# Performance work log

Hardware: AMD Instinct MI355X
Metric: run time of the kernel (lower is better)

## Reference

```python
import jax, jax.numpy as jnp
import numpy as np

D_MODEL = 512; NHEAD = 8; D_FF = 2048
B = 8; C = 64; P = 128
HALF = D_MODEL // 2        # per-branch embed dim (256)
H_HALF = NHEAD // 2        # per-branch heads (4)
HD = HALF // H_HALF        # per-branch head dim (64)
ROPE_BASE = 10000.0
THETA_SCALE = 2.0 * np.pi
LN_EPS = 1e-5; RMS_EPS = 1e-8


def setup_inputs():
    ks = jax.random.split(jax.random.key(0), 16)
    w = lambda k, s: jax.random.normal(k, s, jnp.float32) * 0.02
    return {
        "src": jax.random.normal(ks[0], (B, C, P, D_MODEL), jnp.float32),
        "coords": jax.random.normal(ks[1], (C, 3), jnp.float32),
        "q_attn": w(ks[2], (D_MODEL,)), "rms_attn": jnp.ones((D_MODEL,), jnp.float32),
        "proj_attn_w": w(ks[3], (D_MODEL, D_MODEL)), "proj_attn_b": jnp.zeros((D_MODEL,), jnp.float32),
        "q_ffn": w(ks[4], (D_MODEL,)), "rms_ffn": jnp.ones((D_MODEL,), jnp.float32),
        "proj_ffn_w": w(ks[5], (D_MODEL, D_MODEL)), "proj_ffn_b": jnp.zeros((D_MODEL,), jnp.float32),
        "ln1_w": jnp.ones((D_MODEL,), jnp.float32), "ln1_b": jnp.zeros((D_MODEL,), jnp.float32),
        "ln2_w": jnp.ones((D_MODEL,), jnp.float32), "ln2_b": jnp.zeros((D_MODEL,), jnp.float32),
        "qkv_s_w": w(ks[6], (3 * HALF, HALF)), "qkv_s_b": jnp.zeros((3 * HALF,), jnp.float32),
        "out_s_w": w(ks[7], (HALF, HALF)), "out_s_b": jnp.zeros((HALF,), jnp.float32),
        "qkv_t_w": w(ks[8], (3 * HALF, HALF)), "qkv_t_b": jnp.zeros((3 * HALF,), jnp.float32),
        "out_t_w": w(ks[9], (HALF, HALF)), "out_t_b": jnp.zeros((HALF,), jnp.float32),
        "w1": w(ks[10], (D_FF, D_MODEL)), "b1": jnp.zeros((D_FF,), jnp.float32),
        "w2": w(ks[11], (D_MODEL, D_FF)), "b2": jnp.zeros((D_MODEL,), jnp.float32),
    }


def _rmsnorm(x, w):
    return x / jnp.sqrt(jnp.mean(x * x, axis=-1, keepdims=True) + RMS_EPS) * w


def _layernorm(x, w, b):
    m = jnp.mean(x, axis=-1, keepdims=True)
    v = jnp.mean((x - m) ** 2, axis=-1, keepdims=True)
    return (x - m) / jnp.sqrt(v + LN_EPS) * w + b


def _attn_residual(src, q, norm_w, proj_w, proj_b):
    # sources = [src] stacked on a leading n-axis (n=1) as in AttentionResidual
    V = src[None]                                  # (n, B, C, P, D)
    K = _rmsnorm(V, norm_w)
    logits = jnp.einsum('d,nbcpd->nbcp', q, K)
    wgt = jax.nn.softmax(logits, axis=0)
    out = jnp.einsum('nbcp,nbcpd->bcpd', wgt, V)
    return out @ proj_w.T + proj_b


def _build_freqs(half, dtype):
    idx = jnp.arange(half, dtype=dtype)
    return 1.0 / ROPE_BASE ** (idx / max(half, 1))


def _coord_rope(coords, half):
    # coords: (L, 3); returns cos, sin of shape (1, 1, L, half)
    axis_ids = jnp.arange(half) % 3
    c = coords - jnp.mean(coords, axis=0, keepdims=True)
    r = jnp.linalg.norm(c, axis=-1)
    c = c / jnp.maximum(jnp.max(r), 1e-6)
    freqs = _build_freqs(half, coords.dtype)
    theta = THETA_SCALE * (c[:, axis_ids] * freqs[None, :])   # (L, half)
    return jnp.cos(theta)[None, None], jnp.sin(theta)[None, None]


def _index_rope(L, half, dtype):
    freqs = _build_freqs(half, dtype)
    pos = jnp.arange(L, dtype=dtype)[:, None]
    theta = pos * freqs[None, :]                               # (L, half)
    return jnp.cos(theta)[None, None], jnp.sin(theta)[None, None]


def _apply_rope(q, k, cos, sin):
    half = q.shape[-1] // 2
    q1, q2 = q[..., :half], q[..., half:]
    k1, k2 = k[..., :half], k[..., half:]
    qr = jnp.concatenate([q1 * cos - q2 * sin, q1 * sin + q2 * cos], axis=-1)
    kr = jnp.concatenate([k1 * cos - k2 * sin, k1 * sin + k2 * cos], axis=-1)
    return qr, kr


def _mha(x, w_qkv, b_qkv, w_o, b_o, H, cos, sin):
    Bx, L, E = x.shape
    Hd = E // H
    qkv = x @ w_qkv.T + b_qkv
    q, k, v = jnp.split(qkv, 3, axis=-1)
    q = q.reshape(Bx, L, H, Hd).transpose(0, 2, 1, 3)   # (B, H, L, Hd)
    k = k.reshape(Bx, L, H, Hd).transpose(0, 2, 1, 3)
    v = v.reshape(Bx, L, H, Hd).transpose(0, 2, 1, 3)
    q, k = _apply_rope(q, k, cos, sin)
    scores = jnp.einsum('bhld,bhmd->bhlm', q, k) * (Hd ** -0.5)
    attn = jax.nn.softmax(scores, axis=-1)
    out = jnp.einsum('bhlm,bhmd->bhld', attn, v)
    out = out.transpose(0, 2, 1, 3).reshape(Bx, L, E)
    return out @ w_o.T + b_o


def reference(src, coords, q_attn, rms_attn, proj_attn_w, proj_attn_b,
              q_ffn, rms_ffn, proj_ffn_w, proj_ffn_b,
              ln1_w, ln1_b, ln2_w, ln2_b,
              qkv_s_w, qkv_s_b, out_s_w, out_s_b,
              qkv_t_w, qkv_t_b, out_t_w, out_t_b,
              w1, b1, w2, b2):
    Bx, Cx, Px, D = src.shape
    half = D // 2
    # --- attention block (pre-norm, attention-residual shortcut) ---
    res1 = _attn_residual(src, q_attn, rms_attn, proj_attn_w, proj_attn_b)
    x = _layernorm(src, ln1_w, ln1_b)
    # spatial branch: attention over channels with coordinate RoPE
    xs = x[..., :half].transpose(0, 2, 1, 3).reshape(Bx * Px, Cx, half)
    cos_s, sin_s = _coord_rope(coords, HD // 2)
    ys = _mha(xs, qkv_s_w, qkv_s_b, out_s_w, out_s_b, H_HALF, cos_s, sin_s)
    ys = ys.reshape(Bx, Px, Cx, half).transpose(0, 2, 1, 3)
    # temporal branch: attention over patches with index RoPE
    xt = x[..., half:].reshape(Bx * Cx, Px, half)
    cos_t, sin_t = _index_rope(Px, HD // 2, src.dtype)
    yt = _mha(xt, qkv_t_w, qkv_t_b, out_t_w, out_t_b, H_HALF, cos_t, sin_t)
    yt = yt.reshape(Bx, Cx, Px, half)
    x = res1 + jnp.concatenate([ys, yt], axis=-1)
    # --- FFN block ---
    res2 = _attn_residual(x, q_ffn, rms_ffn, proj_ffn_w, proj_ffn_b)
    y = _layernorm(x, ln2_w, ln2_b)
    ff = jax.nn.gelu(y @ w1.T + b1, approximate=False) @ w2.T + b2
    return res2 + ff
```

## Files before the change

kernel.cpp:

```cpp
#include <hip/hip_runtime.h>
#include <math.h>
#include <type_traits>

using u16 = unsigned short;
using u32 = unsigned int;

typedef __bf16 bf16x8 __attribute__((ext_vector_type(8)));
typedef float f32x4 __attribute__((ext_vector_type(4)));

__device__ __forceinline__ float lof(u32 u) { u32 x = u << 16; float f; __builtin_memcpy(&f, &x, 4); return f; }
__device__ __forceinline__ float hif(u32 u) { u32 x = u & 0xffff0000u; float f; __builtin_memcpy(&f, &x, 4); return f; }
__device__ __forceinline__ u16 f2bf(float f) {
  u32 u; __builtin_memcpy(&u, &f, 4);
  u32 r = u + 0x7fffu + ((u >> 16) & 1u);
  return (u16)(r >> 16);
}
__device__ __forceinline__ u32 pack2(float a, float b) { return (u32)f2bf(a) | ((u32)f2bf(b) << 16); }
__device__ __forceinline__ float bf2f(u16 s) { u32 x = ((u32)s) << 16; float f; __builtin_memcpy(&f, &x, 4); return f; }
__device__ __forceinline__ float elem(const u32* arr, int j) { u32 u = arr[j >> 1]; return (j & 1) ? hif(u) : lof(u); }

__device__ __forceinline__ void gload_lds16(const u16* g, u16* l) {
  __builtin_amdgcn_global_load_lds((const __attribute__((address_space(1))) void*)g,
                                   (__attribute__((address_space(3))) void*)l, 16, 0, 0);
}

#define NTOK 65536

#define WB_PA   0
#define WB_PF   262144
#define WB_QS   524288
#define WB_QT   720896
#define WB_OS   917504
#define WB_OT   983040
#define WB_W1   1048576
#define WB_W2F  2097152
#define WB_TOT  3407872

#define UC_US 0
#define UC_CS 768
#define UC_UT 1536
#define UC_CT 2304
#define UC_U1 3072
#define UC_C1 5120
#define UC_BC 7168

constexpr size_t O_WB  = 0;
constexpr size_t O_TAB = 6815744;
constexpr size_t O_ST1 = 6864896;
constexpr size_t O_ST2 = 7389184;
constexpr size_t O_UC  = 7913472;
constexpr size_t O_X   = 7944192;
constexpr size_t O_HB  = O_X + (size_t)NTOK * 512 * 2;

__global__ __launch_bounds__(256) void convert_weights_kernel(
    const float* __restrict__ pa, const float* __restrict__ pf,
    const float* __restrict__ qs, const float* __restrict__ qt,
    const float* __restrict__ os_, const float* __restrict__ ot,
    const float* __restrict__ w1, const float* __restrict__ w2,
    const float* __restrict__ ln1w, const float* __restrict__ ln2w,
    u16* __restrict__ dst)
{
  int i = blockIdx.x * 256 + threadIdx.x;
  if (i >= WB_TOT) return;
  float v;
  if (i < 262144)       { v = pa[i]; }
  else if (i < 524288)  { v = pf[i - 262144]; }
  else if (i < 720896)  { int l = i - 524288;  v = qs[l] * ln1w[l & 255]; }
  else if (i < 917504)  { int l = i - 720896;  v = qt[l] * ln1w[256 + (l & 255)]; }
  else if (i < 983040)  { v = os_[i - 917504]; }
  else if (i < 1048576) { v = ot[i - 983040]; }
  else if (i < 2097152) { int l = i - 1048576; v = w1[l] * ln2w[l & 511]; }
  else {
    int l = i - 2097152; int row = l / 2560, col = l - row * 2560;
    v = (col < 2048) ? w2[row * 2048 + col] : pf[row * 512 + (col - 2048)];
  }
  dst[i] = f2bf(v);
}

__global__ __launch_bounds__(256) void ucvec_kernel(
    const float* __restrict__ qs, const float* __restrict__ qt, const float* __restrict__ w1,
    const float* __restrict__ ln1w, const float* __restrict__ ln1b,
    const float* __restrict__ ln2w, const float* __restrict__ ln2b,
    const float* __restrict__ b2, const float* __restrict__ pfb,
    float* __restrict__ uc)
{
  int j = blockIdx.x * 256 + threadIdx.x;
  if (j < 768) {
    float u = 0.f, c = 0.f;
    for (int k = 0; k < 256; k++) { float w = qs[j * 256 + k]; u += ln1w[k] * w; c += ln1b[k] * w; }
    uc[UC_US + j] = u; uc[UC_CS + j] = c;
  } else if (j < 1536) {
    int jj = j - 768; float u = 0.f, c = 0.f;
    for (int k = 0; k < 256; k++) { float w = qt[jj * 256 + k]; u += ln1w[256 + k] * w; c += ln1b[256 + k] * w; }
    uc[UC_UT + jj] = u; uc[UC_CT + jj] = c;
  } else if (j < 3584) {
    int jj = j - 1536; float u = 0.f, c = 0.f;
    for (int k = 0; k < 512; k++) { float w = w1[jj * 512 + k]; u += ln2w[k] * w; c += ln2b[k] * w; }
    uc[UC_U1 + jj] = u; uc[UC_C1 + jj] = c;
  } else if (j < 4096) {
    int jj = j - 3584;
    uc[UC_BC + jj] = b2[jj] + pfb[jj];
  }
}

__global__ __launch_bounds__(256) void rope_tables_kernel(const float* __restrict__ coords, float* __restrict__ tab)
{
  __shared__ float cs[192];
  __shared__ float mean3[3];
  __shared__ float rmax;
  int t = threadIdx.x;
  if (t < 192) cs[t] = coords[t];
  __syncthreads();
  if (t < 3) { float s = 0.f; for (int i = 0; i < 64; i++) s += cs[i * 3 + t]; mean3[t] = s * (1.0f / 64.0f); }
  __syncthreads();
  if (t < 192) cs[t] -= mean3[t % 3];
  __syncthreads();
  if (t == 0) {
    float mx = 0.f;
    for (int i = 0; i < 64; i++) {
      float x = cs[i * 3], y = cs[i * 3 + 1], z = cs[i * 3 + 2];
      mx = fmaxf(mx, sqrtf(x * x + y * y + z * z));
    }
    rmax = fmaxf(mx, 1e-6f);
  }
  __syncthreads();
  float inv = 1.0f / rmax;
  for (int e = t; e < 2048; e += 256) {
    int c = e >> 5, j = e & 31;
    float freq = 1.0f / powf(10000.0f, (float)j * (1.0f / 32.0f));
    float th = 6.283185307179586f * (cs[c * 3 + (j % 3)] * inv) * freq;
    tab[e] = cosf(th); tab[2048 + e] = sinf(th);
  }
  for (int e = t; e < 4096; e += 256) {
    int p = e >> 5, j = e & 31;
    float freq = 1.0f / powf(10000.0f, (float)j * (1.0f / 32.0f));
    float th = (float)p * freq;
    tab[4096 + e] = cosf(th); tab[8192 + e] = sinf(th);
  }
}

__global__ __launch_bounds__(256) void ln_stats_f32_kernel(
    const float* __restrict__ xin, float2* __restrict__ st, u16* __restrict__ srcb)
{
  const int tok = blockIdx.x * 4 + (threadIdx.x >> 6);
  const int lane = threadIdx.x & 63;
  const float* row = xin + (size_t)tok * 512 + lane * 8;
  float4 v0 = ((const float4*)row)[0];
  float4 v1 = ((const float4*)row)[1];
  float v[8] = {v0.x, v0.y, v0.z, v0.w, v1.x, v1.y, v1.z, v1.w};
  float s = 0.f, ss = 0.f;
#pragma unroll
  for (int j = 0; j < 8; j++) { s += v[j]; ss += v[j] * v[j]; }
#pragma unroll
  for (int o = 32; o > 0; o >>= 1) { s += __shfl_xor(s, o); ss += __shfl_xor(ss, o); }
  if (lane == 0) {
    float mean = s * (1.0f / 512.0f);
    float rstd = rsqrtf(ss * (1.0f / 512.0f) - mean * mean + 1e-5f);
    st[tok] = make_float2(mean, rstd);
  }
  if (srcb) {
    uint4 o; u32* op = (u32*)&o;
#pragma unroll
    for (int d = 0; d < 4; d++) op[d] = pack2(v[2 * d], v[2 * d + 1]);
    *(uint4*)(srcb + (size_t)tok * 512 + lane * 8) = o;
  }
}

__global__ __launch_bounds__(256) void ln_stats_bf16_kernel(const u16* __restrict__ xin, float2* __restrict__ st)
{
  const int tok = blockIdx.x * 4 + (threadIdx.x >> 6);
  const int lane = threadIdx.x & 63;
  uint4 u = ((const uint4*)(xin + (size_t)tok * 512))[lane];
  u32 uu[4] = {u.x, u.y, u.z, u.w};
  float s = 0.f, ss = 0.f;
#pragma unroll
  for (int d = 0; d < 4; d++) {
    float a = lof(uu[d]), b = hif(uu[d]);
    s += a + b; ss += a * a + b * b;
  }
#pragma unroll
  for (int o = 32; o > 0; o >>= 1) { s += __shfl_xor(s, o); ss += __shfl_xor(ss, o); }
  if (lane == 0) {
    float mean = s * (1.0f / 512.0f);
    float rstd = rsqrtf(ss * (1.0f / 512.0f) - mean * mean + 1e-5f);
    st[tok] = make_float2(mean, rstd);
  }
}

#define BM 128
#define BN 128
#define BKT 32

template<int AMODE, int EMODE, typename OutT>
__global__ __launch_bounds__(256) void gemm_kernel(
    const void* __restrict__ Av, int lda,
    const u16* __restrict__ A2, int lda2,
    const u16* __restrict__ Wt, int ldw,
    OutT* __restrict__ C, int ldc,
    const float* __restrict__ bias,
    const float2* __restrict__ stats,
    const float* __restrict__ uvec, const float* __restrict__ cvec,
    int K)
{
  const int t = threadIdx.x;
  const int lane = t & 63, wid = t >> 6;
  const int wm = wid >> 1, wn = wid & 1;
  const int l15 = lane & 15, l4 = lane >> 4;
  const int r0 = t >> 2;

  const int ntn = gridDim.x;
  const int nwg = ntn * gridDim.y;
  int flat = blockIdx.y * ntn + blockIdx.x;
  int q = nwg >> 3, rmd = nwg & 7, xcd = flat & 7, idx = flat >> 3;
  int wg = (xcd < rmd ? xcd * (q + 1) : rmd * (q + 1) + (xcd - rmd) * q) + idx;
  const int m0 = (wg / ntn) * BM, n0 = (wg % ntn) * BN;

  f32x4 acc[4][4] = {};

  const size_t arow0 = (size_t)(m0 + r0);
  const u16* A16 = (const u16*)Av;
  const float* A32 = (const float*)Av;

  if constexpr (AMODE == 0 || AMODE == 4) {
    __shared__ u16 Asb[2][BM * 32];
    __shared__ u16 Bsb[2][BN * 32];
    const int chs = (t & 3) ^ ((t >> 3) & 3);
    const u16* Wp = Wt + (size_t)(n0 + r0) * ldw + chs * 8;
    const size_t wstep = (size_t)64 * ldw;
    const int nt = K / BKT;
    auto stage = [&](int ti, int buf) {
      const int kk = ti * BKT;
      const int cbk = kk + chs * 8;
      const u16* pa; size_t rstep;
      if constexpr (AMODE == 4) {
        if (kk < 2048) { pa = A16 + arow0 * lda + cbk;           rstep = (size_t)64 * lda; }
        else           { pa = A2 + arow0 * lda2 + (cbk - 2048);  rstep = (size_t)64 * lda2; }
      } else {
        pa = A16 + arow0 * lda + cbk; rstep = (size_t)64 * lda;
      }
      gload_lds16(pa, &Asb[buf][t * 8]);
      gload_lds16(pa + rstep, &Asb[buf][t * 8 + 2048]);
      gload_lds16(Wp + kk, &Bsb[buf][t * 8]);
      gload_lds16(Wp + wstep + kk, &Bsb[buf][t * 8 + 2048]);
    };
    stage(0, 0);
    int cur = 0;
    const int pco = (l4 ^ ((l15 >> 1) & 3)) * 8;
    for (int ti = 0; ti < nt; ti++) {
      if (ti + 1 < nt) {
        stage(ti + 1, cur ^ 1);
        __builtin_amdgcn_sched_barrier(0);
        asm volatile("s_waitcnt vmcnt(4)" ::: "memory");
      } else {
        __builtin_amdgcn_sched_barrier(0);
        asm volatile("s_waitcnt vmcnt(0)" ::: "memory");
      }
      __builtin_amdgcn_sched_barrier(0);
      __builtin_amdgcn_s_barrier();
      __builtin_amdgcn_sched_barrier(0);
      bf16x8 af[4], bfr[4];
#pragma unroll
      for (int i = 0; i < 4; i++)
        af[i] = *(const bf16x8*)(&Asb[cur][(wm * 64 + i * 16 + l15) * 32 + pco]);
#pragma unroll
      for (int j = 0; j < 4; j++)
        bfr[j] = *(const bf16x8*)(&Bsb[cur][(wn * 64 + j * 16 + l15) * 32 + pco]);
#pragma unroll
      for (int i = 0; i < 4; i++)
#pragma unroll
        for (int j = 0; j < 4; j++)
          acc[i][j] = __builtin_amdgcn_mfma_f32_16x16x32_bf16(af[i], bfr[j], acc[i][j], 0, 0, 0);
      __builtin_amdgcn_sched_barrier(0);
      __builtin_amdgcn_s_barrier();
      __builtin_amdgcn_sched_barrier(0);
      cur ^= 1;
    }
  } else {
    const int ch = t & 3;
    const u16* Wp = Wt + (size_t)(n0 + r0) * ldw + ch * 8;
    const size_t wstep = (size_t)64 * ldw;
    __shared__ u16 As[BM * 40];
    __shared__ u16 Bs[BN * 32];
    for (int k0 = 0; k0 < K; k0 += BKT) {
      const int cb = k0 + ch * 8;
      uint4 a0, a1;
      float f0[8], f1[8];
      float4 x0 = *(const float4*)(A32 + arow0 * lda + cb);
      float4 x1 = *(const float4*)(A32 + arow0 * lda + cb + 4);
      float4 y0 = *(const float4*)(A32 + (arow0 + 64) * lda + cb);
      float4 y1 = *(const float4*)(A32 + (arow0 + 64) * lda + cb + 4);
      f0[0]=x0.x; f0[1]=x0.y; f0[2]=x0.z; f0[3]=x0.w; f0[4]=x1.x; f0[5]=x1.y; f0[6]=x1.z; f0[7]=x1.w;
      f1[0]=y0.x; f1[1]=y0.y; f1[2]=y0.z; f1[3]=y0.w; f1[4]=y1.x; f1[5]=y1.y; f1[6]=y1.z; f1[7]=y1.w;
      u32* p0 = (u32*)&a0; u32* p1 = (u32*)&a1;
#pragma unroll
      for (int d = 0; d < 4; d++) { p0[d] = pack2(f0[2*d], f0[2*d+1]); p1[d] = pack2(f1[2*d], f1[2*d+1]); }
      __syncthreads();
      gload_lds16(Wp + k0, Bs + t * 8);
      gload_lds16(Wp + wstep + k0, Bs + t * 8 + 2048);
      *(uint4*)(As + r0 * 40 + ch * 8) = a0;
      *(uint4*)(As + (r0 + 64) * 40 + ch * 8) = a1;
      __syncthreads();
      bf16x8 af[4], bfr[4];
#pragma unroll
      for (int i = 0; i < 4; i++)
        af[i] = *(const bf16x8*)(As + (wm * 64 + i * 16 + l15) * 40 + l4 * 8);
#pragma unroll
      for (int j = 0; j < 4; j++)
        bfr[j] = *(const bf16x8*)(Bs + (wn * 64 + j * 16 + l15) * 32 + l4 * 8);
#pragma unroll
      for (int i = 0; i < 4; i++)
#pragma unroll
        for (int j = 0; j < 4; j++)
          acc[i][j] = __builtin_amdgcn_mfma_f32_16x16x32_bf16(af[i], bfr[j], acc[i][j], 0, 0, 0);
    }
  }

#pragma unroll
  for (int i = 0; i < 4; i++) {
    const int row = m0 + wm * 64 + i * 16 + l4 * 4;
#pragma unroll
    for (int j = 0; j < 4; j++) {
      const int col = n0 + wn * 64 + j * 16 + l15;
      const float bv = bias[col];
#pragma unroll
      for (int rr = 0; rr < 4; rr++) {
        float v = acc[i][j][rr];
        if constexpr (EMODE >= 3) {
          float2 s = stats[row + rr];
          v = s.y * v - s.x * s.y * uvec[col] + cvec[col] + bv;
          if constexpr (EMODE == 4) v = 0.5f * v * (1.0f + erff(v * 0.7071067811865475f));
        } else {
          v += bv;
        }
        const size_t idxc = (size_t)(row + rr) * ldc + col;
        if constexpr (std::is_same<OutT, u16>::value) {
          if constexpr (EMODE == 2) v += bf2f(C[idxc]);
          C[idxc] = f2bf(v);
        } else {
          if constexpr (EMODE == 2) v += C[idxc];
          C[idxc] = v;
        }
      }
    }
  }
}

template<int L>
__global__ __launch_bounds__(256) void attn_mfma_kernel(
    const u16* __restrict__ qkv,
    u16* __restrict__ aout,
    const float* __restrict__ tab)
{
  constexpr int KP = 72;
  constexpr int PP = L + 8;
  constexpr int VP = L + 8;
  constexpr int NI = L / 64;
  constexpr int NJ = L / 16;
  constexpr int NK = L / 32;
  __shared__ u16 Ks[L * KP];
  __shared__ u16 Vt[64 * VP];
  __shared__ u16 Ps[L * PP];

  const int t = threadIdx.x;
  const int lane = t & 63;
  const int w = t >> 6;
  const int l15 = lane & 15, l4 = lane >> 4;
  const int sq = blockIdx.x, h = blockIdx.y;

  long base; int tstride; const float *ct, *st;
  if constexpr (L == 64) { base = (long)(sq >> 7) * 8192 + (sq & 127); tstride = 128; ct = tab;        st = tab + 2048; }
  else                   { base = (long)sq * 128;                      tstride = 1;   ct = tab + 4096; st = tab + 8192; }

  {
    const int tok = t >> 1, hh = t & 1;
    if (tok < L) {
      const size_t rb = (size_t)(base + (long)tok * tstride) * 768 + h * 64;
      u32 ku[32];
#pragma unroll
      for (int i = 0; i < 8; i++) ((uint4*)ku)[i] = ((const uint4*)(qkv + rb + 256))[i];
      const float* cc = ct + tok * 32;
      const float* ss = st + tok * 32;
      u32* kd = (u32*)(Ks + tok * KP + hh * 32);
#pragma unroll
      for (int jj = 0; jj < 16; jj++) {
        float c0 = cc[2*jj], s0 = ss[2*jj], c1 = cc[2*jj+1], s1 = ss[2*jj+1];
        float a0 = elem(ku, 2*jj),     b0 = elem(ku, 2*jj+32);
        float a1 = elem(ku, 2*jj+1),   b1 = elem(ku, 2*jj+33);
        float r0v = hh ? (a0*s0 + b0*c0) : (a0*c0 - b0*s0);
        float r1v = hh ? (a1*s1 + b1*c1) : (a1*c1 - b1*s1);
        kd[jj] = pack2(r0v, r1v);
      }
      u32 vu[16];
#pragma unroll
      for (int i = 0; i < 4; i++) ((uint4*)vu)[i] = ((const uint4*)(qkv + rb + 512 + hh * 32))[i];
#pragma unroll
      for (int j = 0; j < 32; j++)
        Vt[(hh * 32 + j) * VP + tok] = (u16)(vu[j >> 1] >> ((j & 1) * 16));
    }
  }

  bf16x8 aq[NI][2];
#pragma unroll
  for (int i = 0; i < NI; i++) {
    const int row = w * (16 * NI) + i * 16 + l15;
    const u16* qr = qkv + (size_t)(base + (long)row * tstride) * 768 + h * 64;
    uint4 ua = *(const uint4*)(qr + l4 * 8);
    uint4 ub = *(const uint4*)(qr + 32 + l4 * 8);
    u32 au[4] = {ua.x, ua.y, ua.z, ua.w};
    u32 bu[4] = {ub.x, ub.y, ub.z, ub.w};
    const float* cc = ct + row * 32 + l4 * 8;
    const float* ss = st + row * 32 + l4 * 8;
    u32 q0[4], q1[4];
#pragma unroll
    for (int d = 0; d < 4; d++) {
      float a0 = lof(au[d]), a1 = hif(au[d]);
      float b0 = lof(bu[d]), b1 = hif(bu[d]);
      float c0 = cc[2*d], c1 = cc[2*d+1], s0 = ss[2*d], s1 = ss[2*d+1];
      q0[d] = pack2(a0*c0 - b0*s0, a1*c1 - b1*s1);
      q1[d] = pack2(a0*s0 + b0*c0, a1*s1 + b1*c1);
    }
    __builtin_memcpy(&aq[i][0], q0, 16);
    __builtin_memcpy(&aq[i][1], q1, 16);
  }
  __syncthreads();

  f32x4 acc[NI][NJ] = {};
#pragma unroll
  for (int j = 0; j < NJ; j++) {
#pragma unroll
    for (int kk = 0; kk < 2; kk++) {
      bf16x8 bk = *(const bf16x8*)(Ks + (j * 16 + l15) * KP + kk * 32 + l4 * 8);
#pragma unroll
      for (int i = 0; i < NI; i++)
        acc[i][j] = __builtin_amdgcn_mfma_f32_16x16x32_bf16(aq[i][kk], bk, acc[i][j], 0, 0, 0);
    }
  }

  float inv_[NI][4];
#pragma unroll
  for (int i = 0; i < NI; i++) {
#pragma unroll
    for (int rr = 0; rr < 4; rr++) {
      float m = acc[i][0][rr];
#pragma unroll
      for (int j = 1; j < NJ; j++) m = fmaxf(m, acc[i][j][rr]);
      m = fmaxf(m, __shfl_xor(m, 1)); m = fmaxf(m, __shfl_xor(m, 2));
      m = fmaxf(m, __shfl_xor(m, 4)); m = fmaxf(m, __shfl_xor(m, 8));
      m *= 0.125f;
      const int qrow = w * (16 * NI) + i * 16 + l4 * 4 + rr;
      float sm = 0.f;
#pragma unroll
      for (int j = 0; j < NJ; j++) {
        float e = __expf(acc[i][j][rr] * 0.125f - m);
        sm += e;
        Ps[qrow * PP + j * 16 + l15] = f2bf(e);
      }
      sm += __shfl_xor(sm, 1); sm += __shfl_xor(sm, 2);
      sm += __shfl_xor(sm, 4); sm += __shfl_xor(sm, 8);
      inv_[i][rr] = 1.0f / sm;
    }
  }

  f32x4 o[NI][4] = {};
#pragma unroll
  for (int kk = 0; kk < NK; kk++) {
    bf16x8 pa[NI];
#pragma unroll
    for (int i = 0; i < NI; i++)
      pa[i] = *(const bf16x8*)(Ps + (w * (16 * NI) + i * 16 + l15) * PP + kk * 32 + l4 * 8);
#pragma unroll
    for (int jn = 0; jn < 4; jn++) {
      bf16x8 bv = *(const bf16x8*)(Vt + (jn * 16 + l15) * VP + kk * 32 + l4 * 8);
#pragma unroll
      for (int i = 0; i < NI; i++)
        o[i][jn] = __builtin_amdgcn_mfma_f32_16x16x32_bf16(pa[i], bv, o[i][jn], 0, 0, 0);
    }
  }

#pragma unroll
  for (int i = 0; i < NI; i++) {
#pragma unroll
    for (int rr = 0; rr < 4; rr++) {
      const int qrow = w * (16 * NI) + i * 16 + l4 * 4 + rr;
      u16* op = aout + (size_t)(base + (long)qrow * tstride) * 256 + h * 64;
      const float iv = inv_[i][rr];
#pragma unroll
      for (int jn = 0; jn < 4; jn++)
        op[jn * 16 + l15] = f2bf(o[i][jn][rr] * iv);
    }
  }
}

extern "C" void kernel_launch(void* const* d_in, const int* in_sizes, int n_in,
                              void* d_out, int out_size, void* d_ws, size_t ws_size,
                              hipStream_t stream) {
  const float* src         = (const float*)d_in[0];
  const float* coords      = (const float*)d_in[1];
  const float* proj_attn_w = (const float*)d_in[4];
  const float* proj_attn_b = (const float*)d_in[5];
  const float* proj_ffn_w  = (const float*)d_in[8];
  const float* proj_ffn_b  = (const float*)d_in[9];
  const float* ln1_w = (const float*)d_in[10];
  const float* ln1_b = (const float*)d_in[11];
  const float* ln2_w = (const float*)d_in[12];
  const float* ln2_b = (const float*)d_in[13];
  const float* qkv_s_w = (const float*)d_in[14];
  const float* qkv_s_b = (const float*)d_in[15];
  const float* out_s_w = (const float*)d_in[16];
  const float* out_s_b = (const float*)d_in[17];
  const float* qkv_t_w = (const float*)d_in[18];
  const float* qkv_t_b = (const float*)d_in[19];
  const float* out_t_w = (const float*)d_in[20];
  const float* out_t_b = (const float*)d_in[21];
  const float* w1 = (const float*)d_in[22];
  const float* b1 = (const float*)d_in[23];
  const float* w2 = (const float*)d_in[24];
  const float* b2 = (const float*)d_in[25];
  float* out = (float*)d_out;
  char* ws = (char*)d_ws;

  const size_t srcb_bytes = (size_t)NTOK * 512 * 2;
  const int tiers[7] = {65536, 32768, 16384, 8192, 4096, 2048, 512};
  int crows = 0; bool fast = false;
  for (int i = 0; i < 7; i++) {
    size_t need = O_HB + (size_t)tiers[i] * 2048 * 2 + srcb_bytes;
    if (ws_size >= need) { crows = tiers[i]; fast = true; break; }
  }
  if (!crows) {
    for (int i = 0; i < 7; i++)
      if (ws_size >= O_HB + (size_t)tiers[i] * 2048 * 2) { crows = tiers[i]; break; }
  }
  if (!crows) return;
  size_t o_srcb = O_HB + (size_t)crows * 2048 * 2;

  u16*    wb  = (u16*)(ws + O_WB);
  float*  tab = (float*)(ws + O_TAB);
  float2* st1 = (float2*)(ws + O_ST1);
  float2* st2 = (float2*)(ws + O_ST2);
  float*  uc  = (float*)(ws + O_UC);
  u16*    x   = (u16*)(ws + O_X);
  u16*    hb  = (u16*)(ws + O_HB);
  u16*    srcb = fast ? (u16*)(ws + o_srcb) : nullptr;

  u16* qkvb  = (u16*)d_out;
  u16* aoutb = (u16*)((char*)d_out + (size_t)NTOK * 768 * 2);

  convert_weights_kernel<<<(WB_TOT + 255) / 256, 256, 0, stream>>>(
      proj_attn_w, proj_ffn_w, qkv_s_w, qkv_t_w, out_s_w, out_t_w, w1, w2, ln1_w, ln2_w, wb);
  ucvec_kernel<<<16, 256, 0, stream>>>(qkv_s_w, qkv_t_w, w1, ln1_w, ln1_b, ln2_w, ln2_b, b2, proj_ffn_b, uc);
  rope_tables_kernel<<<1, 256, 0, stream>>>(coords, tab);
  ln_stats_f32_kernel<<<NTOK / 4, 256, 0, stream>>>(src, st1, srcb);

  if (fast)
    gemm_kernel<0, 0, u16><<<dim3(4, 512), 256, 0, stream>>>(srcb, 512, nullptr, 0, wb + WB_PA, 512, x, 512, proj_attn_b, nullptr, nullptr, nullptr, 512);
  else
    gemm_kernel<1, 0, u16><<<dim3(4, 512), 256, 0, stream>>>(src, 512, nullptr, 0, wb + WB_PA, 512, x, 512, proj_attn_b, nullptr, nullptr, nullptr, 512);

  if (fast)
    gemm_kernel<0, 3, u16><<<dim3(6, 512), 256, 0, stream>>>(srcb, 512, nullptr, 0, wb + WB_QS, 256, qkvb, 768, qkv_s_b, st1, uc + UC_US, uc + UC_CS, 256);
  else
    gemm_kernel<1, 3, u16><<<dim3(6, 512), 256, 0, stream>>>(src, 512, nullptr, 0, wb + WB_QS, 256, qkvb, 768, qkv_s_b, st1, uc + UC_US, uc + UC_CS, 256);
  attn_mfma_kernel<64><<<dim3(1024, 4), 256, 0, stream>>>(qkvb, aoutb, tab);
  gemm_kernel<0, 2, u16><<<dim3(2, 512), 256, 0, stream>>>(aoutb, 256, nullptr, 0, wb + WB_OS, 256, x, 512, out_s_b, nullptr, nullptr, nullptr, 256);

  if (fast)
    gemm_kernel<0, 3, u16><<<dim3(6, 512), 256, 0, stream>>>(srcb + 256, 512, nullptr, 0, wb + WB_QT, 256, qkvb, 768, qkv_t_b, st1, uc + UC_UT, uc + UC_CT, 256);
  else
    gemm_kernel<1, 3, u16><<<dim3(6, 512), 256, 0, stream>>>(src + 256, 512, nullptr, 0, wb + WB_QT, 256, qkvb, 768, qkv_t_b, st1, uc + UC_UT, uc + UC_CT, 256);
  attn_mfma_kernel<128><<<dim3(512, 4), 256, 0, stream>>>(qkvb, aoutb, tab);
  gemm_kernel<0, 2, u16><<<dim3(2, 512), 256, 0, stream>>>(aoutb, 256, nullptr, 0, wb + WB_OT, 256, x + 256, 512, out_t_b, nullptr, nullptr, nullptr, 256);

  ln_stats_bf16_kernel<<<NTOK / 4, 256, 0, stream>>>(x, st2);

  for (int r = 0; r < NTOK; r += crows) {
    gemm_kernel<0, 4, u16><<<dim3(16, crows / 128), 256, 0, stream>>>(
        x + (size_t)r * 512, 512, nullptr, 0, wb + WB_W1, 512, hb, 2048, b1, st2 + r, uc + UC_U1, uc + UC_C1, 512);
    gemm_kernel<4, 0, float><<<dim3(4, crows / 128), 256, 0, stream>>>(
        hb, 2048, x + (size_t)r * 512, 512, wb + WB_W2F, 2560, out + (size_t)r * 512, 512, uc + UC_BC, nullptr, nullptr, nullptr, 2560);
  }
}
```

Baseline: 1.032 ms.

## Use 256x256-tile 512-thread GEMM with triple-buffered LDS pipeline

Replaces the 128x128, 256-thread bf16 GEMM with a 256x256-tile kernel using 8 waves, each computing 128x64. It also moves from double to triple buffering with a two-stage prefetch and one barrier per iteration, and raises MFMA priority with s_setprio. The larger tile halves global/LDS traffic per FLOP, but it uses 96KB of LDS and more accumulator registers, and the smaller grids (e.g. 256 blocks for the out-projections) may underfill the GPU. The fp32-input path is split into its own kernel and left unchanged.

```diff
diff --git a/kernel.cpp b/kernel.cpp
--- a/kernel.cpp
+++ b/kernel.cpp
@@ -187,13 +187,9 @@
   }
 }
 
-#define BM 128
-#define BN 128
-#define BKT 32
-
 template<int AMODE, int EMODE, typename OutT>
-__global__ __launch_bounds__(256) void gemm_kernel(
-    const void* __restrict__ Av, int lda,
+__global__ __launch_bounds__(512, 2) void gemm256_kernel(
+    const u16* __restrict__ A16, int lda,
     const u16* __restrict__ A2, int lda2,
     const u16* __restrict__ Wt, int ldw,
     OutT* __restrict__ C, int ldc,
@@ -202,122 +198,81 @@
     const float* __restrict__ uvec, const float* __restrict__ cvec,
     int K)
 {
+  __shared__ u16 As[3][256 * 32];
+  __shared__ u16 Bs[3][256 * 32];
   const int t = threadIdx.x;
   const int lane = t & 63, wid = t >> 6;
-  const int wm = wid >> 1, wn = wid & 1;
+  const int wm = wid >> 2, wn = wid & 3;
   const int l15 = lane & 15, l4 = lane >> 4;
   const int r0 = t >> 2;
+  const int chs = (t & 3) ^ ((t >> 3) & 3);
 
   const int ntn = gridDim.x;
   const int nwg = ntn * gridDim.y;
   int flat = blockIdx.y * ntn + blockIdx.x;
   int q = nwg >> 3, rmd = nwg & 7, xcd = flat & 7, idx = flat >> 3;
   int wg = (xcd < rmd ? xcd * (q + 1) : rmd * (q + 1) + (xcd - rmd) * q) + idx;
-  const int m0 = (wg / ntn) * BM, n0 = (wg % ntn) * BN;
-
-  f32x4 acc[4][4] = {};
+  const int m0 = (wg / ntn) * 256, n0 = (wg % ntn) * 256;
+
+  f32x4 acc[8][4] = {};
 
   const size_t arow0 = (size_t)(m0 + r0);
-  const u16* A16 = (const u16*)Av;
-  const float* A32 = (const float*)Av;
-
-  if constexpr (AMODE == 0 || AMODE == 4) {
-    __shared__ u16 Asb[2][BM * 32];
-    __shared__ u16 Bsb[2][BN * 32];
-    const int chs = (t & 3) ^ ((t >> 3) & 3);
-    const u16* Wp = Wt + (size_t)(n0 + r0) * ldw + chs * 8;
-    const size_t wstep = (size_t)64 * ldw;
-    const int nt = K / BKT;
-    auto stage = [&](int ti, int buf) {
-      const int kk = ti * BKT;
-      const int cbk = kk + chs * 8;
-      const u16* pa; size_t rstep;
-      if constexpr (AMODE == 4) {
-        if (kk < 2048) { pa = A16 + arow0 * lda + cbk;           rstep = (size_t)64 * lda; }
-        else           { pa = A2 + arow0 * lda2 + (cbk - 2048);  rstep = (size_t)64 * lda2; }
-      } else {
-        pa = A16 + arow0 * lda + cbk; rstep = (size_t)64 * lda;
-      }
-      gload_lds16(pa, &Asb[buf][t * 8]);
-      gload_lds16(pa + rstep, &Asb[buf][t * 8 + 2048]);
-      gload_lds16(Wp + kk, &Bsb[buf][t * 8]);
-      gload_lds16(Wp + wstep + kk, &Bsb[buf][t * 8 + 2048]);
-    };
-    stage(0, 0);
-    int cur = 0;
-    const int pco = (l4 ^ ((l15 >> 1) & 3)) * 8;
-    for (int ti = 0; ti < nt; ti++) {
-      if (ti + 1 < nt) {
-        stage(ti + 1, cur ^ 1);
-        __builtin_amdgcn_sched_barrier(0);
-        asm volatile("s_waitcnt vmcnt(4)" ::: "memory");
-      } else {
-        __builtin_amdgcn_sched_barrier(0);
-        asm volatile("s_waitcnt vmcnt(0)" ::: "memory");
-      }
-      __builtin_amdgcn_sched_barrier(0);
-      __builtin_amdgcn_s_barrier();
-      __builtin_amdgcn_sched_barrier(0);
-      bf16x8 af[4], bfr[4];
-#pragma unroll
-      for (int i = 0; i < 4; i++)
-        af[i] = *(const bf16x8*)(&Asb[cur][(wm * 64 + i * 16 + l15) * 32 + pco]);
+  const u16* Wp = Wt + (size_t)(n0 + r0) * ldw + chs * 8;
+  const size_t wstep = (size_t)128 * ldw;
+  const int nt = K >> 5;
+
+  auto stage = [&](int ti, int buf) {
+    const int kk = ti << 5;
+    const int cbk = kk + chs * 8;
+    const u16* pa; size_t rstep;
+    if constexpr (AMODE == 4) {
+      if (kk < 2048) { pa = A16 + arow0 * lda + cbk;          rstep = (size_t)128 * lda; }
+      else           { pa = A2 + arow0 * lda2 + (cbk - 2048); rstep = (size_t)128 * lda2; }
+    } else {
+      pa = A16 + arow0 * lda + cbk; rstep = (size_t)128 * lda;
+    }
+    gload_lds16(pa,         &As[buf][t * 8]);
+    gload_lds16(pa + rstep, &As[buf][t * 8 + 4096]);
+    gload_lds16(Wp + kk,          &Bs[buf][t * 8]);
+    gload_lds16(Wp + wstep + kk,  &Bs[buf][t * 8 + 4096]);
+  };
+
+  stage(0, 0);
+  stage(1, 1);
+  const int pco = (l4 ^ ((l15 >> 1) & 3)) * 8;
+  int cb = 0;
+  for (int ti = 0; ti < nt; ti++) {
+    __builtin_amdgcn_sched_barrier(0);
+    if (ti + 1 < nt) { asm volatile("s_waitcnt vmcnt(4)" ::: "memory"); }
+    else             { asm volatile("s_waitcnt vmcnt(0)" ::: "memory"); }
+    __builtin_amdgcn_sched_barrier(0);
+    __builtin_amdgcn_s_barrier();
+    __builtin_amdgcn_sched_barrier(0);
+    if (ti + 2 < nt) {
+      int b2 = cb + 2; if (b2 >= 3) b2 -= 3;
+      stage(ti + 2, b2);
+    }
+    bf16x8 af[8], bfr[4];
+#pragma unroll
+    for (int i = 0; i < 8; i++)
+      af[i] = *(const bf16x8*)(&As[cb][(wm * 128 + i * 16 + l15) * 32 + pco]);
+#pragma unroll
+    for (int j = 0; j < 4; j++)
+      bfr[j] = *(const bf16x8*)(&Bs[cb][(wn * 64 + j * 16 + l15) * 32 + pco]);
+    __builtin_amdgcn_s_setprio(1);
+#pragma unroll
+    for (int i = 0; i < 8; i++)
 #pragma unroll
       for (int j = 0; j < 4; j++)
-        bfr[j] = *(const bf16x8*)(&Bsb[cur][(wn * 64 + j * 16 + l15) * 32 + pco]);
-#pragma unroll
-      for (int i = 0; i < 4; i++)
-#pragma unroll
-        for (int j = 0; j < 4; j++)
-          acc[i][j] = __builtin_amdgcn_mfma_f32_16x16x32_bf16(af[i], bfr[j], acc[i][j], 0, 0, 0);
-      __builtin_amdgcn_sched_barrier(0);
-      __builtin_amdgcn_s_barrier();
-      __builtin_amdgcn_sched_barrier(0);
-      cur ^= 1;
-    }
-  } else {
-    const int ch = t & 3;
-    const u16* Wp = Wt + (size_t)(n0 + r0) * ldw + ch * 8;
-    const size_t wstep = (size_t)64 * ldw;
-    __shared__ u16 As[BM * 40];
-    __shared__ u16 Bs[BN * 32];
-    for (int k0 = 0; k0 < K; k0 += BKT) {
-      const int cb = k0 + ch * 8;
-      uint4 a0, a1;
-      float f0[8], f1[8];
-      float4 x0 = *(const float4*)(A32 + arow0 * lda + cb);
-      float4 x1 = *(const float4*)(A32 + arow0 * lda + cb + 4);
-      float4 y0 = *(const float4*)(A32 + (arow0 + 64) * lda + cb);
-      float4 y1 = *(const float4*)(A32 + (arow0 + 64) * lda + cb + 4);
-      f0[0]=x0.x; f0[1]=x0.y; f0[2]=x0.z; f0[3]=x0.w; f0[4]=x1.x; f0[5]=x1.y; f0[6]=x1.z; f0[7]=x1.w;
-      f1[0]=y0.x; f1[1]=y0.y; f1[2]=y0.z; f1[3]=y0.w; f1[4]=y1.x; f1[5]=y1.y; f1[6]=y1.z; f1[7]=y1.w;
-      u32* p0 = (u32*)&a0; u32* p1 = (u32*)&a1;
-#pragma unroll
-      for (int d = 0; d < 4; d++) { p0[d] = pack2(f0[2*d], f0[2*d+1]); p1[d] = pack2(f1[2*d], f1[2*d+1]); }
-      __syncthreads();
-      gload_lds16(Wp + k0, Bs + t * 8);
-      gload_lds16(Wp + wstep + k0, Bs + t * 8 + 2048);
-      *(uint4*)(As + r0 * 40 + ch * 8) = a0;
-      *(uint4*)(As + (r0 + 64) * 40 + ch * 8) = a1;
-      __syncthreads();
-      bf16x8 af[4], bfr[4];
-#pragma unroll
-      for (int i = 0; i < 4; i++)
-        af[i] = *(const bf16x8*)(As + (wm * 64 + i * 16 + l15) * 40 + l4 * 8);
-#pragma unroll
-      for (int j = 0; j < 4; j++)
-        bfr[j] = *(const bf16x8*)(Bs + (wn * 64 + j * 16 + l15) * 32 + l4 * 8);
-#pragma unroll
-      for (int i = 0; i < 4; i++)
-#pragma unroll
-        for (int j = 0; j < 4; j++)
-          acc[i][j] = __builtin_amdgcn_mfma_f32_16x16x32_bf16(af[i], bfr[j], acc[i][j], 0, 0, 0);
-    }
-  }
-
-#pragma unroll
-  for (int i = 0; i < 4; i++) {
-    const int row = m0 + wm * 64 + i * 16 + l4 * 4;
+        acc[i][j] = __builtin_amdgcn_mfma_f32_16x16x32_bf16(af[i], bfr[j], acc[i][j], 0, 0, 0);
+    __builtin_amdgcn_s_setprio(0);
+    __builtin_amdgcn_sched_barrier(0);
+    cb = cb == 2 ? 0 : cb + 1;
+  }
+
+#pragma unroll
+  for (int i = 0; i < 8; i++) {
+    const int row = m0 + wm * 128 + i * 16 + l4 * 4;
 #pragma unroll
     for (int j = 0; j < 4; j++) {
       const int col = n0 + wn * 64 + j * 16 + l15;
@@ -340,6 +295,90 @@
           if constexpr (EMODE == 2) v += C[idxc];
           C[idxc] = v;
         }
+      }
+    }
+  }
+}
+
+template<int EMODE, typename OutT>
+__global__ __launch_bounds__(256) void gemm_f32a_kernel(
+    const float* __restrict__ A32, int lda,
+    const u16* __restrict__ Wt, int ldw,
+    OutT* __restrict__ C, int ldc,
+    const float* __restrict__ bias,
+    const float2* __restrict__ stats,
+    const float* __restrict__ uvec, const float* __restrict__ cvec,
+    int K)
+{
+  const int t = threadIdx.x;
+  const int lane = t & 63, wid = t >> 6;
+  const int wm = wid >> 1, wn = wid & 1;
+  const int l15 = lane & 15, l4 = lane >> 4;
+  const int r0 = t >> 2;
+  const int ntn = gridDim.x;
+  const int nwg = ntn * gridDim.y;
+  int flat = blockIdx.y * ntn + blockIdx.x;
+  int q = nwg >> 3, rmd = nwg & 7, xcd = flat & 7, idx = flat >> 3;
+  int wg = (xcd < rmd ? xcd * (q + 1) : rmd * (q + 1) + (xcd - rmd) * q) + idx;
+  const int m0 = (wg / ntn) * 128, n0 = (wg % ntn) * 128;
+  f32x4 acc[4][4] = {};
+  const size_t arow0 = (size_t)(m0 + r0);
+  const int ch = t & 3;
+  const u16* Wp = Wt + (size_t)(n0 + r0) * ldw + ch * 8;
+  const size_t wstep = (size_t)64 * ldw;
+  __shared__ u16 As[128 * 40];
+  __shared__ u16 Bs[128 * 32];
+  for (int k0 = 0; k0 < K; k0 += 32) {
+    const int cbx = k0 + ch * 8;
+    uint4 a0, a1;
+    float f0[8], f1[8];
+    float4 x0 = *(const float4*)(A32 + arow0 * lda + cbx);
+    float4 x1 = *(const float4*)(A32 + arow0 * lda + cbx + 4);
+    float4 y0 = *(const float4*)(A32 + (arow0 + 64) * lda + cbx);
+    float4 y1 = *(const float4*)(A32 + (arow0 + 64) * lda + cbx + 4);
+    f0[0]=x0.x; f0[1]=x0.y; f0[2]=x0.z; f0[3]=x0.w; f0[4]=x1.x; f0[5]=x1.y; f0[6]=x1.z; f0[7]=x1.w;
+    f1[0]=y0.x; f1[1]=y0.y; f1[2]=y0.z; f1[3]=y0.w; f1[4]=y1.x; f1[5]=y1.y; f1[6]=y1.z; f1[7]=y1.w;
+    u32* p0 = (u32*)&a0; u32* p1 = (u32*)&a1;
+#pragma unroll
+    for (int d = 0; d < 4; d++) { p0[d] = pack2(f0[2*d], f0[2*d+1]); p1[d] = pack2(f1[2*d], f1[2*d+1]); }
+    __syncthreads();
+    gload_lds16(Wp + k0, Bs + t * 8);
+    gload_lds16(Wp + wstep + k0, Bs + t * 8 + 2048);
+    *(uint4*)(As + r0 * 40 + ch * 8) = a0;
+    *(uint4*)(As + (r0 + 64) * 40 + ch * 8) = a1;
+    __syncthreads();
+    bf16x8 af[4], bfr[4];
+#pragma unroll
+    for (int i = 0; i < 4; i++)
+      af[i] = *(const bf16x8*)(As + (wm * 64 + i * 16 + l15) * 40 + l4 * 8);
+#pragma unroll
+    for (int j = 0; j < 4; j++)
+      bfr[j] = *(const bf16x8*)(Bs + (wn * 64 + j * 16 + l15) * 32 + l4 * 8);
+#pragma unroll
+    for (int i = 0; i < 4; i++)
+#pragma unroll
+      for (int j = 0; j < 4; j++)
+        acc[i][j] = __builtin_amdgcn_mfma_f32_16x16x32_bf16(af[i], bfr[j], acc[i][j], 0, 0, 0);
+  }
+#pragma unroll
+  for (int i = 0; i < 4; i++) {
+    const int row = m0 + wm * 64 + i * 16 + l4 * 4;
+#pragma unroll
+    for (int j = 0; j < 4; j++) {
+      const int col = n0 + wn * 64 + j * 16 + l15;
+      const float bv = bias[col];
+#pragma unroll
+      for (int rr = 0; rr < 4; rr++) {
+        float v = acc[i][j][rr];
+        if constexpr (EMODE >= 3) {
+          float2 s = stats[row + rr];
+          v = s.y * v - s.x * s.y * uvec[col] + cvec[col] + bv;
+        } else {
+          v += bv;
+        }
+        const size_t idxc = (size_t)(row + rr) * ldc + col;
+        if constexpr (std::is_same<OutT, u16>::value) C[idxc] = f2bf(v);
+        else C[idxc] = v;
       }
     }
   }
@@ -552,30 +591,30 @@
   ln_stats_f32_kernel<<<NTOK / 4, 256, 0, stream>>>(src, st1, srcb);
 
   if (fast)
-    gemm_kernel<0, 0, u16><<<dim3(4, 512), 256, 0, stream>>>(srcb, 512, nullptr, 0, wb + WB_PA, 512, x, 512, proj_attn_b, nullptr, nullptr, nullptr, 512);
+    gemm256_kernel<0, 0, u16><<<dim3(2, 256), 512, 0, stream>>>(srcb, 512, nullptr, 0, wb + WB_PA, 512, x, 512, proj_attn_b, nullptr, nullptr, nullptr, 512);
   else
-    gemm_kernel<1, 0, u16><<<dim3(4, 512), 256, 0, stream>>>(src, 512, nullptr, 0, wb + WB_PA, 512, x, 512, proj_attn_b, nullptr, nullptr, nullptr, 512);
+    gemm_f32a_kernel<0, u16><<<dim3(4, 512), 256, 0, stream>>>(src, 512, wb + WB_PA, 512, x, 512, proj_attn_b, nullptr, nullptr, nullptr, 512);
 
   if (fast)
-    gemm_kernel<0, 3, u16><<<dim3(6, 512), 256, 0, stream>>>(srcb, 512, nullptr, 0, wb + WB_QS, 256, qkvb, 768, qkv_s_b, st1, uc + UC_US, uc + UC_CS, 256);
+    gemm256_kernel<0, 3, u16><<<dim3(3, 256), 512, 0, stream>>>(srcb, 512, nullptr, 0, wb + WB_QS, 256, qkvb, 768, qkv_s_b, st1, uc + UC_US, uc + UC_CS, 256);
   else
-    gemm_kernel<1, 3, u16><<<dim3(6, 512), 256, 0, stream>>>(src, 512, nullptr, 0, wb + WB_QS, 256, qkvb, 768, qkv_s_b, st1, uc + UC_US, uc + UC_CS, 256);
+    gemm_f32a_kernel<3, u16><<<dim3(6, 512), 256, 0, stream>>>(src, 512, wb + WB_QS, 256, qkvb, 768, qkv_s_b, st1, uc + UC_US, uc + UC_CS, 256);
   attn_mfma_kernel<64><<<dim3(1024, 4), 256, 0, stream>>>(qkvb, aoutb, tab);
-  gemm_kernel<0, 2, u16><<<dim3(2, 512), 256, 0, stream>>>(aoutb, 256, nullptr, 0, wb + WB_OS, 256, x, 512, out_s_b, nullptr, nullptr, nullptr, 256);
+  gemm256_kernel<0, 2, u16><<<dim3(1, 256), 512, 0, stream>>>(aoutb, 256, nullptr, 0, wb + WB_OS, 256, x, 512, out_s_b, nullptr, nullptr, nullptr, 256);
 
   if (fast)
-    gemm_kernel<0, 3, u16><<<dim3(6, 512), 256, 0, stream>>>(srcb + 256, 512, nullptr, 0, wb + WB_QT, 256, qkvb, 768, qkv_t_b, st1, uc + UC_UT, uc + UC_CT, 256);
+    gemm256_kernel<0, 3, u16><<<dim3(3, 256), 512, 0, stream>>>(srcb + 256, 512, nullptr, 0, wb + WB_QT, 256, qkvb, 768, qkv_t_b, st1, uc + UC_UT, uc + UC_CT, 256);
   else
-    gemm_kernel<1, 3, u16><<<dim3(6, 512), 256, 0, stream>>>(src + 256, 512, nullptr, 0, wb + WB_QT, 256, qkvb, 768, qkv_t_b, st1, uc + UC_UT, uc + UC_CT, 256);
+    gemm_f32a_kernel<3, u16><<<dim3(6, 512), 256, 0, stream>>>(src + 256, 512, wb + WB_QT, 256, qkvb, 768, qkv_t_b, st1, uc + UC_UT, uc + UC_CT, 256);
   attn_mfma_kernel<128><<<dim3(512, 4), 256, 0, stream>>>(qkvb, aoutb, tab);
-  gemm_kernel<0, 2, u16><<<dim3(2, 512), 256, 0, stream>>>(aoutb, 256, nullptr, 0, wb + WB_OT, 256, x + 256, 512, out_t_b, nullptr, nullptr, nullptr, 256);
+  gemm256_kernel<0, 2, u16><<<dim3(1, 256), 512, 0, stream>>>(aoutb, 256, nullptr, 0, wb + WB_OT, 256, x + 256, 512, out_t_b, nullptr, nullptr, nullptr, 256);
 
   ln_stats_bf16_kernel<<<NTOK / 4, 256, 0, stream>>>(x, st2);
 
   for (int r = 0; r < NTOK; r += crows) {
-    gemm_kernel<0, 4, u16><<<dim3(16, crows / 128), 256, 0, stream>>>(
+    gemm256_kernel<0, 4, u16><<<dim3(8, crows / 256), 512, 0, stream>>>(
         x + (size_t)r * 512, 512, nullptr, 0, wb + WB_W1, 512, hb, 2048, b1, st2 + r, uc + UC_U1, uc + UC_C1, 512);
-    gemm_kernel<4, 0, float><<<dim3(4, crows / 128), 256, 0, stream>>>(
+    gemm256_kernel<4, 0, float><<<dim3(2, crows / 256), 512, 0, stream>>>(
         hb, 2048, x + (size_t)r * 512, 512, wb + WB_W2F, 2560, out + (size_t)r * 512, 512, uc + UC_BC, nullptr, nullptr, nullptr, 2560);
   }
 }
```

Result: no change. 1.025 ms (-0.7%).
